# Kernel optimization log

Measured on AMD Instinct MI355X. Metric: run time of the kernel, lower is better.

The kernel has to match this reference:

```python
import jax, jax.numpy as jnp
import numpy as np

HEAD_NUM = 16
NEG_BIG = -2.0**32 + 1.0


def _pos_encoding(T, D):
    pos = np.arange(T)[:, None].astype(np.float64)
    i = np.arange(D)[None, :].astype(np.float64)
    angle = pos / np.power(10000.0, 2.0 * i / D)
    pe = np.empty((T, D), dtype=np.float64)
    pe[:, 0::2] = np.sin(angle[:, 0::2])
    pe[:, 1::2] = np.cos(angle[:, 1::2])
    return jnp.asarray(pe * (D ** 0.5), dtype=jnp.float32)  # scale=True


def setup_inputs() -> dict:
    key = jax.random.key(0)
    ks = jax.random.split(key, 9)
    B, T, D = 32, 512, 1024
    return {
        "queries": jax.random.normal(ks[0], (B, T, D), jnp.float32),
        "keys": jax.random.normal(ks[1], (B, T, D), jnp.float32),
        "query_masks": jax.random.randint(ks[2], (B, 1), 1, T + 1, jnp.int32),
        "key_masks": jax.random.randint(ks[3], (B, 1), 1, T + 1, jnp.int32),
        "W_Query": jax.random.normal(ks[4], (D, D), jnp.float32) * 0.02,
        "W_key": jax.random.normal(ks[5], (D, D), jnp.float32) * 0.02,
        "W_Value": jax.random.normal(ks[6], (D, D), jnp.float32) * 0.02,
        "fw1": jax.random.normal(ks[7], (D, 4 * D), jnp.float32) * 0.02,
        "fw2": jax.random.normal(ks[8], (4 * D, D), jnp.float32) * 0.02,
    }


def reference(queries, keys, query_masks, key_masks, W_Query, W_key, W_Value, fw1, fw2):
    B, T, D = queries.shape
    h = HEAD_NUM
    d = D // h
    pe = _pos_encoding(T, D)  # [T, D]

    # faithful to source: queries get PE; keys = PE(queries_with_PE) (keys input unused)
    q_pe = queries + pe[None]
    k_pe = q_pe + pe[None]

    qs = jnp.einsum('btd,de->bte', q_pe, W_Query)
    ks_ = jnp.einsum('btd,de->bte', k_pe, W_key)
    vs = jnp.einsum('btd,de->bte', ks_, W_Value)  # faithful: values from projected keys

    def split_heads(x):  # [B,T,h*d] -> [h,B,T,d] (matches tf.split/concat on axis 0)
        return x.reshape(B, T, h, d).transpose(2, 0, 1, 3)

    q4, k4, v4 = split_heads(qs), split_heads(ks_), split_heads(vs)

    scores = jnp.einsum('hbqd,hbkd->hbqk', q4, k4) / (d ** 0.5)

    pos = jnp.arange(T)
    km = (pos[None, :] < key_masks).astype(jnp.float32)    # [B,T]
    qm = (pos[None, :] < query_masks).astype(jnp.float32)  # [B,T]

    scores = jnp.where(km[None, :, None, :] == 1.0, scores, NEG_BIG)
    scores = scores - jnp.max(scores, axis=-1, keepdims=True)
    attn = jax.nn.softmax(scores, axis=-1)
    attn = attn * qm[None, :, :, None]

    out = jnp.einsum('hbqk,hbkd->hbqd', attn, v4)
    result = out.transpose(1, 2, 0, 3).reshape(B, T, D)  # merge heads (head-major)

    result = result + q_pe  # use_res
    # feed forward (use_layer_norm=False, no dropout at inference)
    hmid = jax.nn.relu(jnp.einsum('btd,df->btf', result, fw1))
    result = result + jnp.einsum('btf,fd->btd', hmid, fw2)

    # output_type == 'mean'
    return jnp.mean(result, axis=1, keepdims=True)  # [B,1,D]
```

## Files before the change

### kernel.cpp

```cpp
#include <hip/hip_runtime.h>

constexpr int B_  = 32;
constexpr int T_  = 512;
constexpr int D_  = 1024;
constexpr int NH_ = 16;
constexpr int DH_ = 64;
constexpr int F_  = 4096;
constexpr int BT_ = B_ * T_;

typedef __attribute__((ext_vector_type(8))) short bf16x8;
typedef __attribute__((ext_vector_type(4))) float f32x4;

#define DEVI __device__ __forceinline__

DEVI unsigned short f2bf(float f) {
  union { float f; unsigned u; } uf; uf.f = f;
  unsigned r = uf.u + 0x7fffu + ((uf.u >> 16) & 1u);
  return (unsigned short)(r >> 16);
}
DEVI float b2f(unsigned short h) {
  union { unsigned u; float f; } uf; uf.u = ((unsigned)h) << 16;
  return uf.f;
}
DEVI void gload16(const void* g, void* l) {
  __builtin_amdgcn_global_load_lds(
      (const __attribute__((address_space(1))) void*)(uintptr_t)g,
      (__attribute__((address_space(3))) void*)(unsigned)(uintptr_t)l, 16, 0, 0);
}

__global__ void pe_kernel(float* __restrict__ pe) {
  int idx = blockIdx.x * 256 + threadIdx.x;
  int t = idx >> 10, j = idx & 1023;
  float inv = exp2f(-(2.0f * (float)j / 1024.0f) * 13.2877123795494f);
  float ang = (float)t * inv;
  float v = (j & 1) ? cosf(ang) : sinf(ang);
  pe[idx] = v * 32.0f;
}

__global__ void pack_kernel(const float* __restrict__ q, const float* __restrict__ pe,
                            unsigned short* __restrict__ q_pe, unsigned short* __restrict__ k_pe) {
  long i = ((long)blockIdx.x * 256 + threadIdx.x) * 4;
  const float4 qv = *(const float4*)(q + i);
  const float4 pv = *(const float4*)(pe + (i & (long)(T_ * D_ - 1)));
  ushort4 a, b;
  a.x = f2bf(qv.x + pv.x); a.y = f2bf(qv.y + pv.y);
  a.z = f2bf(qv.z + pv.z); a.w = f2bf(qv.w + pv.w);
  b.x = f2bf(qv.x + 2.f * pv.x); b.y = f2bf(qv.y + 2.f * pv.y);
  b.z = f2bf(qv.z + 2.f * pv.z); b.w = f2bf(qv.w + 2.f * pv.w);
  *(ushort4*)(q_pe + i) = a;
  *(ushort4*)(k_pe + i) = b;
}

__global__ void prep_w(const float* __restrict__ Wq, const float* __restrict__ Wk,
                       const float* __restrict__ Wv, const float* __restrict__ fw1,
                       unsigned short* __restrict__ Wqt, unsigned short* __restrict__ Wkt,
                       unsigned short* __restrict__ Wvt, unsigned short* __restrict__ fw1t,
                       unsigned short* __restrict__ Wkbf) {
  const int z = blockIdx.z;
  if (z < 3 && blockIdx.x >= 32) return;
  const float* W = (z == 0) ? Wq : (z == 1) ? Wk : (z == 2) ? Wv : fw1;
  unsigned short* Wt = (z == 0) ? Wqt : (z == 1) ? Wkt : (z == 2) ? Wvt : fw1t;
  const int N = (z == 3) ? F_ : D_;
  __shared__ float tile[32][33];
  int tx = threadIdx.x & 31, ty = threadIdx.x >> 5;
  int bx = blockIdx.x, by = blockIdx.y;
  for (int i = 0; i < 4; i++) {
    int r = by * 32 + ty + i * 8;
    float v = W[(long)r * N + bx * 32 + tx];
    tile[ty + i * 8][tx] = v;
    if (z == 1) Wkbf[(long)r * D_ + bx * 32 + tx] = f2bf(v);
  }
  __syncthreads();
  for (int i = 0; i < 4; i++) {
    int r = bx * 32 + ty + i * 8;
    Wt[(long)r * D_ + by * 32 + tx] = f2bf(tile[tx][ty + i * 8]);
  }
}

template <int EPI>
__global__ __launch_bounds__(256) void gemm_bt(
    const unsigned short* __restrict__ A0, const unsigned short* __restrict__ Bt0,
    unsigned short* __restrict__ C0, float* __restrict__ hacc, int M, int N, int K) {
  __shared__ unsigned short As[128 * 32];
  __shared__ unsigned short Bs[128 * 32];
  const unsigned short* A  = A0;
  const unsigned short* Bt = Bt0;
  unsigned short* C        = C0;

  const int tid = threadIdx.x;
  const int lane = tid & 63, w = tid >> 6;
  const int wr = w >> 1, wc = w & 1;
  const int l15 = lane & 15, lhi = lane >> 4;
  const int brow = blockIdx.y * 128, bcol = blockIdx.x * 128;

  f32x4 acc[4][4] = {};
  const int o = tid * 16;
  const int srow = o >> 6;
  const int skel = (o & 63) >> 1;

  for (int kk = 0; kk < K; kk += 32) {
    gload16(A + (long)(brow + srow) * K + kk + skel,        (char*)As + o);
    gload16(A + (long)(brow + srow + 64) * K + kk + skel,   (char*)As + o + 4096);
    gload16(Bt + (long)(bcol + srow) * K + kk + skel,       (char*)Bs + o);
    gload16(Bt + (long)(bcol + srow + 64) * K + kk + skel,  (char*)Bs + o + 4096);
    __syncthreads();
    bf16x8 af[4], bfr[4];
    for (int m = 0; m < 4; m++)
      af[m] = *(const bf16x8*)((const char*)As + ((wr * 64 + m * 16 + l15) * 64 + lhi * 16));
    for (int n = 0; n < 4; n++)
      bfr[n] = *(const bf16x8*)((const char*)Bs + ((wc * 64 + n * 16 + l15) * 64 + lhi * 16));
    for (int m = 0; m < 4; m++)
      for (int n = 0; n < 4; n++)
        acc[m][n] = __builtin_amdgcn_mfma_f32_16x16x32_bf16(af[m], bfr[n], acc[m][n], 0, 0, 0);
    __syncthreads();
  }

  for (int m = 0; m < 4; m++)
    for (int n = 0; n < 4; n++) {
      int row = brow + wr * 64 + m * 16 + lhi * 4;
      int col = bcol + wc * 64 + n * 16 + l15;
      for (int r = 0; r < 4; r++)
        C[(long)(row + r) * N + col] = f2bf(acc[m][n][r]);
    }
}

template <int EPI, int GSWAP>
__global__ __launch_bounds__(512, 2) void gemm8(
    const unsigned short* __restrict__ A0, const unsigned short* __restrict__ Bt0, unsigned short* __restrict__ C0,
    const unsigned short* __restrict__ A1, const unsigned short* __restrict__ Bt1, unsigned short* __restrict__ C1,
    const unsigned short* __restrict__ A2, const unsigned short* __restrict__ Bt2, unsigned short* __restrict__ C2,
    float* __restrict__ hacc, int N,
    const int* __restrict__ L0, const int* __restrict__ L1, const int* __restrict__ L2) {
  constexpr int K = 1024, NK = 16, NI = 8;
  __shared__ char lds[2][2][32768];

  const int z = blockIdx.z;
  const unsigned short* A  = (z == 0) ? A0  : (z == 1 ? A1  : A2);
  const unsigned short* Bt = (z == 0) ? Bt0 : (z == 1 ? Bt1 : Bt2);
  unsigned short* C        = (z == 0) ? C0  : (z == 1 ? C1  : C2);
  const int* L             = (z == 0) ? L0  : (z == 1 ? L1  : L2);

  const long brow = (long)(GSWAP ? blockIdx.y : blockIdx.x) * 256;
  const long bcol = (long)(GSWAP ? blockIdx.x : blockIdx.y) * 256;
  if (L && (brow & 256) && L[brow >> 9] <= 256) return;

  const int tid = threadIdx.x;
  const int lane = tid & 63, w = tid >> 6;
  const int wm = w >> 2, wn = w & 3;
  const int l15 = lane & 15, lhi = lane >> 4;

  const int drow = (tid * 16) >> 7;
  const int dcol = ((tid * 16) & 127) ^ ((drow & 7) << 4);
  const int sw   = (l15 & 7) << 4;

  f32x4 acc[8][4] = {};
  bf16x8 bfr[4][2], af[2][2];

  auto STAGE = [&](const unsigned short* __restrict__ P, long tb, int kt, int h, int buf, int op) {
    const unsigned short* g = P + (tb + h * 128 + drow) * (long)K + kt * 64 + (dcol >> 1);
    char* l = &lds[buf][op][h * 16384 + tid * 16];
    gload16(g, l);
    gload16(g + 64L * K, l + 8192);
  };
  auto LDA = [&](int buf, int q) {
#pragma unroll
    for (int mi = 0; mi < 2; mi++) {
      int row = wm * 128 + (q * 2 + mi) * 16 + l15;
#pragma unroll
      for (int kk = 0; kk < 2; kk++)
        af[mi][kk] = *(const bf16x8*)(&lds[buf][0][0] + (row << 7) + ((kk * 64 + lhi * 16) ^ sw));
    }
  };
  auto LDB = [&](int buf) {
#pragma unroll
    for (int n = 0; n < 4; n++) {
      int row = wn * 64 + n * 16 + l15;
#pragma unroll
      for (int kk = 0; kk < 2; kk++)
        bfr[n][kk] = *(const bf16x8*)(&lds[buf][1][0] + (row << 7) + ((kk * 64 + lhi * 16) ^ sw));
    }
  };
  auto MFMAQ = [&](int q) {
    __builtin_amdgcn_s_setprio(1);
#pragma unroll
    for (int mi = 0; mi < 2; mi++)
#pragma unroll
      for (int n = 0; n < 4; n++)
#pragma unroll
        for (int kk = 0; kk < 2; kk++)
          acc[q * 2 + mi][n] =
              __builtin_amdgcn_mfma_f32_16x16x32_bf16(af[mi][kk], bfr[n][kk], acc[q * 2 + mi][n], 0, 0, 0);
    __builtin_amdgcn_s_setprio(0);
  };
#define BAR() __builtin_amdgcn_s_barrier()
#define GATE4() asm volatile("s_waitcnt vmcnt(4)" ::: "memory")

  STAGE(A, brow, 0, 0, 0, 0);  STAGE(A, brow, 0, 1, 0, 0);
  STAGE(Bt, bcol, 0, 0, 0, 1); STAGE(Bt, bcol, 0, 1, 0, 1);
  STAGE(Bt, bcol, 1, 0, 1, 1); STAGE(Bt, bcol, 1, 1, 1, 1);
  GATE4();
  BAR();

  for (int i = 0; i < NI; ++i) {
    const int k1 = 2 * i + 1;
    const int ka = (2 * i + 2) & (NK - 1);
    const int kb = (2 * i + 3) & (NK - 1);
    LDA(0, 0); LDB(0); STAGE(A, brow, k1, 0, 1, 0);
    BAR(); MFMAQ(0); BAR();
    LDA(0, 1);         STAGE(A, brow, k1, 1, 1, 0);
    BAR(); MFMAQ(1); BAR();
    LDA(0, 2);         STAGE(Bt, bcol, ka, 0, 0, 1);
    BAR(); MFMAQ(2); BAR();
    LDA(0, 3);         STAGE(Bt, bcol, ka, 1, 0, 1);
    BAR(); MFMAQ(3);
    GATE4();
    BAR();
    LDA(1, 0); LDB(1); STAGE(A, brow, ka, 0, 0, 0);
    BAR(); MFMAQ(0); BAR();
    LDA(1, 1);         STAGE(A, brow, ka, 1, 0, 0);
    BAR(); MFMAQ(1); BAR();
    LDA(1, 2);         STAGE(Bt, bcol, kb, 0, 1, 1);
    BAR(); MFMAQ(2); BAR();
    LDA(1, 3);         STAGE(Bt, bcol, kb, 1, 1, 1);
    BAR(); MFMAQ(3);
    GATE4();
    BAR();
  }
#undef BAR
#undef GATE4

  if (EPI == 0) {
    if (z == 2) {
      asm volatile("s_waitcnt vmcnt(0)" ::: "memory");
      __builtin_amdgcn_s_barrier();
      char* tl = &lds[0][0][0] + (w << 14);
#pragma unroll
      for (int m = 0; m < 8; m++)
#pragma unroll
        for (int n = 0; n < 4; n++) {
          int cl = n * 16 + l15;
#pragma unroll
          for (int r = 0; r < 4; r++) {
            int tofs = m * 16 + lhi * 4 + r;
            *(unsigned short*)(tl + cl * 256 + ((tofs * 2) ^ ((cl & 7) << 4))) = f2bf(acc[m][n][r]);
          }
        }
      asm volatile("" ::: "memory");
      const int bb = (int)(brow >> 9), t0 = (int)(brow & 511);
#pragma unroll
      for (int rr = 0; rr < 16; rr++) {
        int row = rr * 4 + lhi;
        bf16x8 v = *(const bf16x8*)(tl + row * 256 + ((l15 * 16) ^ ((row & 7) << 4)));
        int gcol = (int)bcol + wn * 64 + row;
        long vtrow = ((long)(bb * NH_ + (gcol >> 6))) * DH_ + (gcol & 63);
        *(bf16x8*)(C + vtrow * T_ + t0 + wm * 128 + l15 * 8) = v;
      }
    } else {
#pragma unroll
      for (int m = 0; m < 8; m++)
#pragma unroll
        for (int n = 0; n < 4; n++) {
          long row = brow + wm * 128 + m * 16 + lhi * 4;
          long col = bcol + wn * 64 + n * 16 + l15;
#pragma unroll
          for (int r = 0; r < 4; r++)
            C[(row + r) * (long)N + col] = f2bf(acc[m][n][r]);
        }
    }
  } else {
    const int batch = (int)(brow >> 9);
#pragma unroll
    for (int n = 0; n < 4; n++) {
      float t = 0.f;
#pragma unroll
      for (int m = 0; m < 8; m++)
#pragma unroll
        for (int r = 0; r < 4; r++) t += fmaxf(acc[m][n][r], 0.f);
      t += __shfl_xor(t, 16);
      t += __shfl_xor(t, 32);
      if (lane < 16)
        atomicAdd(hacc + (long)batch * F_ + bcol + wn * 64 + n * 16 + l15, t);
    }
  }
}

__global__ __launch_bounds__(256, 3) void attn_kernel(
    const unsigned short* __restrict__ qs, const unsigned short* __restrict__ ks,
    const unsigned short* __restrict__ vt, const unsigned short* __restrict__ q_pe,
    const int* __restrict__ qmask, const int* __restrict__ kmask,
    unsigned short* __restrict__ res, float* __restrict__ racc) {
  __shared__ unsigned short Ks[2][64 * 64];
  __shared__ unsigned short Vs[2][64 * 64];
  __shared__ unsigned short Ps[4][32 * 64];

  const int tid = threadIdx.x, lane = tid & 63, w = tid >> 6;
  const int l15 = lane & 15, lhi = lane >> 4;
  const int h = blockIdx.x, b = blockIdx.y, q0 = blockIdx.z * 128;
  const int qlen = qmask[b], kvlen = kmask[b];

  if (q0 >= qlen) {
    int cc = tid & 63;
    float s = 0.f;
    for (int i = 0; i < 32; i++) {
      int r = (tid >> 6) * 32 + i;
      long addr = (long)(b * T_ + q0 + r) * D_ + h * DH_ + cc;
      unsigned short v = q_pe[addr];
      res[addr] = v;
      s += b2f(v);
    }
    atomicAdd(racc + b * D_ + h * DH_ + cc, s);
    return;
  }

  bf16x8 qf[2][2];
  for (int m = 0; m < 2; m++)
    for (int k2 = 0; k2 < 2; k2++) {
      int t = q0 + w * 32 + m * 16 + l15;
      qf[m][k2] = *(const bf16x8*)(qs + (long)(b * T_ + t) * D_ + h * DH_ + k2 * 32 + lhi * 8);
    }

  f32x4 o[2][4] = {};
  float mrun[2][4], lrun[2][4];
  for (int m = 0; m < 2; m++)
    for (int r = 0; r < 4; r++) { mrun[m][r] = -3e38f; lrun[m][r] = 0.f; }

  const float SCL = 0.125f * 1.4426950408889634f;
  const float THR = 8.0f / SCL;
  const int nc = (kvlen + 63) >> 6;

  auto stage = [&](int c, int buf) {
#pragma unroll
    for (int cl = 0; cl < 2; cl++) {
      int ob = cl * 4096 + tid * 16;
      int os = ob ^ (((ob >> 7) & 7) << 4);
      int r0 = os >> 7, cb = os & 127;
      gload16(ks + (long)(b * T_ + c * 64 + r0) * D_ + h * DH_ + (cb >> 1),
              (char*)&Ks[buf][0] + ob);
      gload16(vt + ((long)(b * NH_ + h) * DH_ + r0) * T_ + c * 64 + (cb >> 1),
              (char*)&Vs[buf][0] + ob);
    }
  };

  stage(0, 0);
  int cur = 0;
  for (int c = 0; c < nc; c++) {
    const int nxt = (c + 1 < nc) ? c + 1 : c;
    stage(nxt, cur ^ 1);
    asm volatile("s_waitcnt vmcnt(4)" ::: "memory");
    __builtin_amdgcn_sched_barrier(0);
    __builtin_amdgcn_s_barrier();

    f32x4 s[2][4] = {};
    for (int k2 = 0; k2 < 2; k2++)
      for (int n = 0; n < 4; n++) {
        int key = n * 16 + l15;
        int Ab = key * 128 + (k2 * 32 + lhi * 8) * 2;
        bf16x8 kf = *(const bf16x8*)((const char*)&Ks[cur][0] + (Ab ^ ((key & 7) << 4)));
        s[0][n] = __builtin_amdgcn_mfma_f32_16x16x32_bf16(qf[0][k2], kf, s[0][n], 0, 0, 0);
        s[1][n] = __builtin_amdgcn_mfma_f32_16x16x32_bf16(qf[1][k2], kf, s[1][n], 0, 0, 0);
      }

    if (c == nc - 1) {
      for (int n = 0; n < 4; n++)
        if (c * 64 + n * 16 + l15 >= kvlen)
          for (int m = 0; m < 2; m++) s[m][n] = f32x4{-3e38f, -3e38f, -3e38f, -3e38f};
    }

    for (int m = 0; m < 2; m++) {
      float mx[4];
      for (int r = 0; r < 4; r++) {
        float v = s[m][0][r];
        for (int n = 1; n < 4; n++) v = fmaxf(v, s[m][n][r]);
        mx[r] = v;
      }
      for (int msk = 1; msk < 16; msk <<= 1)
        for (int r = 0; r < 4; r++) mx[r] = fmaxf(mx[r], __shfl_xor(mx[r], msk));
      bool grow = false;
      for (int r = 0; r < 4; r++) grow = grow || (mx[r] > mrun[m][r] + THR);
      if (__any(grow)) {
        float corr[4];
        for (int r = 0; r < 4; r++) {
          float mn = fmaxf(mrun[m][r], mx[r]);
          corr[r] = exp2f((mrun[m][r] - mn) * SCL);
          mrun[m][r] = mn;
        }
        for (int nd = 0; nd < 4; nd++)
          for (int r = 0; r < 4; r++) o[m][nd][r] *= corr[r];
        for (int r = 0; r < 4; r++) lrun[m][r] *= corr[r];
      }
      float ps[4] = {0.f, 0.f, 0.f, 0.f};
      for (int n = 0; n < 4; n++)
        for (int r = 0; r < 4; r++) {
          float pval = exp2f((s[m][n][r] - mrun[m][r]) * SCL);
          s[m][n][r] = pval;
          ps[r] += pval;
        }
      for (int msk = 1; msk < 16; msk <<= 1)
        for (int r = 0; r < 4; r++) ps[r] += __shfl_xor(ps[r], msk);
      for (int r = 0; r < 4; r++) lrun[m][r] += ps[r];
      for (int n = 0; n < 4; n++)
        for (int r = 0; r < 4; r++) {
          int row = m * 16 + lhi * 4 + r;
          int Ab = row * 128 + (n * 16 + l15) * 2;
          *(unsigned short*)((char*)&Ps[w][0] + (Ab ^ ((row & 7) << 4))) = f2bf(s[m][n][r]);
        }
    }
    asm volatile("" ::: "memory");

    for (int k4 = 0; k4 < 2; k4++) {
      bf16x8 pa[2];
      for (int m = 0; m < 2; m++) {
        int row = m * 16 + l15;
        int Ab = row * 128 + k4 * 64 + lhi * 16;
        pa[m] = *(const bf16x8*)((const char*)&Ps[w][0] + (Ab ^ ((row & 7) << 4)));
      }
      for (int nd = 0; nd < 4; nd++) {
        int dv = nd * 16 + l15;
        int Ab = dv * 128 + k4 * 64 + lhi * 16;
        bf16x8 vb = *(const bf16x8*)((const char*)&Vs[cur][0] + (Ab ^ ((dv & 7) << 4)));
        for (int m = 0; m < 2; m++)
          o[m][nd] = __builtin_amdgcn_mfma_f32_16x16x32_bf16(pa[m], vb, o[m][nd], 0, 0, 0);
      }
    }
    __builtin_amdgcn_s_barrier();
    cur ^= 1;
  }

  float cs[4] = {0.f, 0.f, 0.f, 0.f};
  for (int m = 0; m < 2; m++)
    for (int r = 0; r < 4; r++) {
      int t = q0 + w * 32 + m * 16 + lhi * 4 + r;
      float inv = 1.0f / lrun[m][r];
      bool valid = t < qlen;
      for (int nd = 0; nd < 4; nd++) {
        long addr = (long)(b * T_ + t) * D_ + h * DH_ + nd * 16 + l15;
        float v = valid ? o[m][nd][r] * inv : 0.f;
        float val = v + b2f(q_pe[addr]);
        res[addr] = f2bf(val);
        cs[nd] += val;
      }
    }
  for (int nd = 0; nd < 4; nd++) {
    cs[nd] += __shfl_xor(cs[nd], 16);
    cs[nd] += __shfl_xor(cs[nd], 32);
  }
  if (lane < 16)
    for (int nd = 0; nd < 4; nd++)
      atomicAdd(racc + b * D_ + h * DH_ + nd * 16 + l15, cs[nd]);
}

__global__ void final_kernel(const float* __restrict__ hacc, const float* __restrict__ fw2,
                             const float* __restrict__ racc, float* __restrict__ out) {
  int n = blockIdx.x * 64 + (threadIdx.x & 63);
  int bg = threadIdx.x >> 6;
  int f0 = blockIdx.y * 512;
  float acc[8] = {};
  for (int f = f0; f < f0 + 512; f++) {
    float wv = fw2[(long)f * D_ + n];
    for (int i = 0; i < 8; i++) acc[i] += hacc[(long)(bg * 8 + i) * F_ + f] * wv;
  }
  if (blockIdx.y == 0)
    for (int i = 0; i < 8; i++) acc[i] += racc[(long)(bg * 8 + i) * D_ + n];
  for (int i = 0; i < 8; i++)
    atomicAdd(out + (bg * 8 + i) * D_ + n, acc[i] * (1.0f / 512.0f));
}

extern "C" void kernel_launch(void* const* d_in, const int* in_sizes, int n_in,
                              void* d_out, int out_size, void* d_ws, size_t ws_size,
                              hipStream_t stream) {
  const float* queries = (const float*)d_in[0];
  const int*   qmask = (const int*)d_in[2];
  const int*   kmask = (const int*)d_in[3];
  const float* Wq  = (const float*)d_in[4];
  const float* Wk  = (const float*)d_in[5];
  const float* Wv  = (const float*)d_in[6];
  const float* fw1 = (const float*)d_in[7];
  const float* fw2 = (const float*)d_in[8];
  float* out = (float*)d_out;

  char* p = (char*)d_ws;
  auto alloc = [&](size_t bytes) -> char* {
    char* r = p; p += (bytes + 255) & ~(size_t)255; return r;
  };
  float*          pe   = (float*)alloc((size_t)T_ * D_ * 4);
  unsigned short* q_pe = (unsigned short*)alloc((size_t)BT_ * D_ * 2);
  unsigned short* k_pe = (unsigned short*)alloc((size_t)BT_ * D_ * 2);
  unsigned short* qs   = (unsigned short*)alloc((size_t)BT_ * D_ * 2);
  unsigned short* ksb  = (unsigned short*)alloc((size_t)BT_ * D_ * 2);
  unsigned short* vt   = (unsigned short*)alloc((size_t)BT_ * D_ * 2);
  unsigned short* res  = (unsigned short*)alloc((size_t)BT_ * D_ * 2);
  unsigned short* Wqt  = (unsigned short*)alloc((size_t)D_ * D_ * 2);
  unsigned short* Wkt  = (unsigned short*)alloc((size_t)D_ * D_ * 2);
  unsigned short* Wvt  = (unsigned short*)alloc((size_t)D_ * D_ * 2);
  unsigned short* Wkbf = (unsigned short*)alloc((size_t)D_ * D_ * 2);
  unsigned short* Wkvt = (unsigned short*)alloc((size_t)D_ * D_ * 2);
  unsigned short* fw1t = (unsigned short*)alloc((size_t)D_ * F_ * 2);
  float*          racc = (float*)alloc((size_t)B_ * D_ * 4);
  float*          hacc = (float*)alloc((size_t)B_ * F_ * 4);

  hipMemsetAsync(hacc, 0, (size_t)B_ * F_ * 4, stream);
  hipMemsetAsync(racc, 0, (size_t)B_ * D_ * 4, stream);
  hipMemsetAsync(out, 0, (size_t)B_ * D_ * 4, stream);

  pe_kernel<<<T_ * D_ / 256, 256, 0, stream>>>(pe);
  pack_kernel<<<BT_ * D_ / 1024, 256, 0, stream>>>(queries, pe, q_pe, k_pe);
  prep_w<<<dim3(128, 32, 4), 256, 0, stream>>>(Wq, Wk, Wv, fw1, Wqt, Wkt, Wvt, fw1t, Wkbf);

  gemm_bt<0><<<dim3(8, 8, 1), 256, 0, stream>>>(Wvt, Wkbf, Wkvt, nullptr, D_, D_, D_);

  gemm8<0, 0><<<dim3(64, 4, 3), 512, 0, stream>>>(q_pe, Wqt, qs,
                                                  k_pe, Wkt, ksb,
                                                  k_pe, Wkvt, vt,
                                                  nullptr, D_, qmask, kmask, kmask);

  attn_kernel<<<dim3(16, 32, 4), 256, 0, stream>>>(qs, ksb, vt, q_pe, qmask, kmask, res, racc);

  gemm8<1, 1><<<dim3(16, 64, 1), 512, 0, stream>>>(res, fw1t, nullptr,
                                                   res, fw1t, nullptr,
                                                   res, fw1t, nullptr,
                                                   hacc, F_, nullptr, nullptr, nullptr);

  final_kernel<<<dim3(16, 8), 256, 0, stream>>>(hacc, fw2, racc, out);
}
```

Baseline: 415.8 us.

## Fuse positional-encoding computation into pack kernel and drop GSWAP grid ordering

Removes the separate pe_kernel and its workspace buffer, computing the sinusoidal positional encoding inline inside pack_kernel for each element. This saves a launch and the read of a 2MB PE table, at the cost of recomputing exp2/sin/cos for every batch element (32x redundant transcendental work). It also removes the GSWAP template option so the FFN gemm launches with row blocks on blockIdx.x, changing block scheduling order and possibly L2 reuse of the fw1 weights.

```diff
diff --git a/kernel.cpp b/kernel.cpp
--- a/kernel.cpp
+++ b/kernel.cpp
@@ -28,25 +28,25 @@
       (__attribute__((address_space(3))) void*)(unsigned)(uintptr_t)l, 16, 0, 0);
 }
 
-__global__ void pe_kernel(float* __restrict__ pe) {
-  int idx = blockIdx.x * 256 + threadIdx.x;
-  int t = idx >> 10, j = idx & 1023;
-  float inv = exp2f(-(2.0f * (float)j / 1024.0f) * 13.2877123795494f);
-  float ang = (float)t * inv;
-  float v = (j & 1) ? cosf(ang) : sinf(ang);
-  pe[idx] = v * 32.0f;
-}
-
-__global__ void pack_kernel(const float* __restrict__ q, const float* __restrict__ pe,
+__global__ void pack_kernel(const float* __restrict__ q,
                             unsigned short* __restrict__ q_pe, unsigned short* __restrict__ k_pe) {
   long i = ((long)blockIdx.x * 256 + threadIdx.x) * 4;
   const float4 qv = *(const float4*)(q + i);
-  const float4 pv = *(const float4*)(pe + (i & (long)(T_ * D_ - 1)));
+  int t = (int)((i >> 10) & 511);
+  int j0 = (int)(i & 1023);
+  float pvv[4];
+#pragma unroll
+  for (int u = 0; u < 4; u++) {
+    int j = j0 + u;
+    float inv = exp2f(-(2.0f * (float)j / 1024.0f) * 13.2877123795494f);
+    float ang = (float)t * inv;
+    pvv[u] = ((j & 1) ? cosf(ang) : sinf(ang)) * 32.0f;
+  }
   ushort4 a, b;
-  a.x = f2bf(qv.x + pv.x); a.y = f2bf(qv.y + pv.y);
-  a.z = f2bf(qv.z + pv.z); a.w = f2bf(qv.w + pv.w);
-  b.x = f2bf(qv.x + 2.f * pv.x); b.y = f2bf(qv.y + 2.f * pv.y);
-  b.z = f2bf(qv.z + 2.f * pv.z); b.w = f2bf(qv.w + 2.f * pv.w);
+  a.x = f2bf(qv.x + pvv[0]); a.y = f2bf(qv.y + pvv[1]);
+  a.z = f2bf(qv.z + pvv[2]); a.w = f2bf(qv.w + pvv[3]);
+  b.x = f2bf(qv.x + 2.f * pvv[0]); b.y = f2bf(qv.y + 2.f * pvv[1]);
+  b.z = f2bf(qv.z + 2.f * pvv[2]); b.w = f2bf(qv.w + 2.f * pvv[3]);
   *(ushort4*)(q_pe + i) = a;
   *(ushort4*)(k_pe + i) = b;
 }
@@ -124,7 +124,7 @@
     }
 }
 
-template <int EPI, int GSWAP>
+template <int EPI>
 __global__ __launch_bounds__(512, 2) void gemm8(
     const unsigned short* __restrict__ A0, const unsigned short* __restrict__ Bt0, unsigned short* __restrict__ C0,
     const unsigned short* __restrict__ A1, const unsigned short* __restrict__ Bt1, unsigned short* __restrict__ C1,
@@ -140,8 +140,7 @@
   unsigned short* C        = (z == 0) ? C0  : (z == 1 ? C1  : C2);
   const int* L             = (z == 0) ? L0  : (z == 1 ? L1  : L2);
 
-  const long brow = (long)(GSWAP ? blockIdx.y : blockIdx.x) * 256;
-  const long bcol = (long)(GSWAP ? blockIdx.x : blockIdx.y) * 256;
+  const long brow = (long)blockIdx.x * 256, bcol = (long)blockIdx.y * 256;
   if (L && (brow & 256) && L[brow >> 9] <= 256) return;
 
   const int tid = threadIdx.x;
@@ -482,7 +481,6 @@
   auto alloc = [&](size_t bytes) -> char* {
     char* r = p; p += (bytes + 255) & ~(size_t)255; return r;
   };
-  float*          pe   = (float*)alloc((size_t)T_ * D_ * 4);
   unsigned short* q_pe = (unsigned short*)alloc((size_t)BT_ * D_ * 2);
   unsigned short* k_pe = (unsigned short*)alloc((size_t)BT_ * D_ * 2);
   unsigned short* qs   = (unsigned short*)alloc((size_t)BT_ * D_ * 2);
@@ -502,23 +500,22 @@
   hipMemsetAsync(racc, 0, (size_t)B_ * D_ * 4, stream);
   hipMemsetAsync(out, 0, (size_t)B_ * D_ * 4, stream);
 
-  pe_kernel<<<T_ * D_ / 256, 256, 0, stream>>>(pe);
-  pack_kernel<<<BT_ * D_ / 1024, 256, 0, stream>>>(queries, pe, q_pe, k_pe);
+  pack_kernel<<<BT_ * D_ / 1024, 256, 0, stream>>>(queries, q_pe, k_pe);
   prep_w<<<dim3(128, 32, 4), 256, 0, stream>>>(Wq, Wk, Wv, fw1, Wqt, Wkt, Wvt, fw1t, Wkbf);
 
   gemm_bt<0><<<dim3(8, 8, 1), 256, 0, stream>>>(Wvt, Wkbf, Wkvt, nullptr, D_, D_, D_);
 
-  gemm8<0, 0><<<dim3(64, 4, 3), 512, 0, stream>>>(q_pe, Wqt, qs,
-                                                  k_pe, Wkt, ksb,
-                                                  k_pe, Wkvt, vt,
-                                                  nullptr, D_, qmask, kmask, kmask);
+  gemm8<0><<<dim3(64, 4, 3), 512, 0, stream>>>(q_pe, Wqt, qs,
+                                               k_pe, Wkt, ksb,
+                                               k_pe, Wkvt, vt,
+                                               nullptr, D_, qmask, kmask, kmask);
 
   attn_kernel<<<dim3(16, 32, 4), 256, 0, stream>>>(qs, ksb, vt, q_pe, qmask, kmask, res, racc);
 
-  gemm8<1, 1><<<dim3(16, 64, 1), 512, 0, stream>>>(res, fw1t, nullptr,
-                                                   res, fw1t, nullptr,
-                                                   res, fw1t, nullptr,
-                                                   hacc, F_, nullptr, nullptr, nullptr);
+  gemm8<1><<<dim3(64, 16, 1), 512, 0, stream>>>(res, fw1t, nullptr,
+                                                res, fw1t, nullptr,
+                                                res, fw1t, nullptr,
+                                                hacc, F_, nullptr, nullptr, nullptr);
 
   final_kernel<<<dim3(16, 8), 256, 0, stream>>>(hacc, fw2, racc, out);
 }
```

After: 409.7 us. No clear change (-1.5%).
